# Kernel optimization log

Hardware: AMD Instinct MI355X
Metric: run time of the kernel (lower is better)

The kernel has to match this reference:

```python
import jax, jax.numpy as jnp
import numpy as np

EPS = 1e-5

def layer_norm(x, gamma, beta):
    mu = jnp.mean(x, axis=-1, keepdims=True)
    var = jnp.var(x, axis=-1, keepdims=True)
    return (x - mu) * jax.lax.rsqrt(var + EPS) * gamma + beta

def setup_inputs() -> dict:
    key = jax.random.key(0)
    ks = jax.random.split(key, 8)
    T, B, E, H, K = 2048, 2, 1024, 16, 64
    x = jax.random.normal(ks[0], (T, B, E), dtype=jnp.float32)
    # causal mask: 0 where allowed (s<=t), -1e9 where masked
    attn_mask = jnp.where(jnp.tril(jnp.ones((T, T), dtype=bool)), 0.0, -1e9).astype(jnp.float32)
    def xavier(k, shape, gain):
        fan_out, fan_in = shape
        std = gain * np.sqrt(2.0 / (fan_in + fan_out))
        return (jax.random.normal(k, shape, dtype=jnp.float32) * std)
    Wq = xavier(ks[1], (H * K, E), 1.0)
    Wk = xavier(ks[2], (K, E), 1.0)
    Wv = xavier(ks[3], (E, E), 1.0)
    return {
        'x': x, 'attn_mask': attn_mask,
        'Wq': Wq, 'bq': jnp.zeros((H * K,), jnp.float32),
        'Wk': Wk, 'bk': jnp.zeros((K,), jnp.float32),
        'Wv': Wv, 'bv': jnp.zeros((E,), jnp.float32),
        'k_gamma': jnp.ones((K,), jnp.float32), 'k_beta': jnp.zeros((K,), jnp.float32),
        'v_gamma': jnp.ones((E,), jnp.float32), 'v_beta': jnp.zeros((E,), jnp.float32),
    }

def reference(x, attn_mask, Wq, bq, Wk, bk, Wv, bv, k_gamma, k_beta, v_gamma, v_beta):
    T, B, E = x.shape
    K = Wk.shape[0]
    H = Wq.shape[0] // K
    q = (x @ Wq.T + bq).reshape(T, B, H, K)          # [T,B,H,K]
    k = layer_norm(x @ Wk.T + bk, k_gamma, k_beta)   # [T,B,K]
    v = layer_norm(x @ Wv.T + bv, v_gamma, v_beta)   # [T,B,E]
    # outer-product state per step, then causal cumulative sum.
    # einsum('ts,sbkd->tbkd', scaling*causal_mask, s) == cumsum over s<=t,
    # scaled per query position t by (t+1)^-0.5 (mask is causal lower-tri).
    outer = jnp.einsum('tbk,tbd->tbkd', k, v)        # [T,B,K,E]
    s = jnp.cumsum(outer, axis=0)
    scaling = jax.lax.rsqrt(jnp.arange(1, T + 1, dtype=x.dtype))
    s = s * scaling[:, None, None, None]
    qn = jnp.mean(jax.nn.softmax(q, axis=-1), axis=2)  # [T,B,K] (dropout_p=0, eval)
    attn = jnp.einsum('tbk,tbkd->tbd', qn, s)          # [T,B,E]
    return attn
```

## Files before the change

kernel.cpp:

```cpp
#include <hip/hip_runtime.h>
#include <math.h>

#define T_DIM 2048
#define B_DIM 2
#define E_DIM 1024
#define K_DIM 64
#define H_DIM 16
#define R_DIM (T_DIM * B_DIM)
#define WROWS 2176
#define NTILE 136

typedef __bf16 bf16x8 __attribute__((ext_vector_type(8)));
typedef __bf16 bf16x4 __attribute__((ext_vector_type(4)));
typedef float f32x4 __attribute__((ext_vector_type(4)));

__global__ __launch_bounds__(256) void cvt_x(const float* __restrict__ X,
                                             __bf16* __restrict__ O) {
    size_t g = ((size_t)blockIdx.x * 256 + threadIdx.x) * 8;
    float4 a = *(const float4*)&X[g];
    float4 b = *(const float4*)&X[g + 4];
    bf16x8 o;
    o[0] = (__bf16)a.x; o[1] = (__bf16)a.y; o[2] = (__bf16)a.z; o[3] = (__bf16)a.w;
    o[4] = (__bf16)b.x; o[5] = (__bf16)b.y; o[6] = (__bf16)b.z; o[7] = (__bf16)b.w;
    *(bf16x8*)&O[g] = o;
}

__global__ __launch_bounds__(256) void cvt_w(const float* __restrict__ Wq,
                                             const float* __restrict__ Wv,
                                             const float* __restrict__ Wk,
                                             __bf16* __restrict__ O) {
    const size_t nq = (size_t)1024 * 1024;
    const size_t nk = (size_t)64 * 1024;
    size_t g = ((size_t)blockIdx.x * 256 + threadIdx.x) * 8;
    bf16x8 o;
    if (g < 2 * nq + nk) {
        const float* src;
        size_t off;
        if (g < nq)          { src = Wq; off = g; }
        else if (g < 2 * nq) { src = Wv; off = g - nq; }
        else                 { src = Wk; off = g - 2 * nq; }
        float4 a = *(const float4*)&src[off];
        float4 b = *(const float4*)&src[off + 4];
        o[0] = (__bf16)a.x; o[1] = (__bf16)a.y; o[2] = (__bf16)a.z; o[3] = (__bf16)a.w;
        o[4] = (__bf16)b.x; o[5] = (__bf16)b.y; o[6] = (__bf16)b.z; o[7] = (__bf16)b.w;
    } else {
#pragma unroll
        for (int i = 0; i < 8; ++i) o[i] = (__bf16)0.f;
    }
    *(bf16x8*)&O[g] = o;
}

__global__ __launch_bounds__(256) void gemm_mfma(const __bf16* __restrict__ XB,
                                                 const __bf16* __restrict__ WB,
                                                 const float* __restrict__ bq,
                                                 const float* __restrict__ bv,
                                                 const float* __restrict__ bk,
                                                 float* __restrict__ Cq,
                                                 float* __restrict__ Cv,
                                                 float* __restrict__ Kr) {
    __shared__ __bf16 Als[128 * 32];
    __shared__ __bf16 Bls[128 * 32];
    const int tid = threadIdx.x;
    const int lane = tid & 63;
    const int w = tid >> 6;
    const int wm = (w & 1) * 64;
    const int wn = (w >> 1) * 64;
    const int rBase = blockIdx.x * 128;
    const int cBase = blockIdx.y * 128;

    const int c0 = tid, c1 = tid + 256;
    const __bf16* gA0 = XB + (size_t)(rBase + (c0 >> 2)) * E_DIM + (c0 & 3) * 8;
    const __bf16* gA1 = XB + (size_t)(rBase + (c1 >> 2)) * E_DIM + (c1 & 3) * 8;
    const __bf16* gB0 = WB + (size_t)(cBase + (c0 >> 2)) * E_DIM + (c0 & 3) * 8;
    const __bf16* gB1 = WB + (size_t)(cBase + (c1 >> 2)) * E_DIM + (c1 & 3) * 8;
    __bf16* lA0 = Als + c0 * 8;
    __bf16* lA1 = Als + c1 * 8;
    __bf16* lB0 = Bls + c0 * 8;
    __bf16* lB1 = Bls + c1 * 8;

    const int fr = lane & 15;
    const int fk = (lane >> 4) * 8;
    const __bf16* aF = Als + (wm + fr) * 32 + fk;
    const __bf16* bF = Bls + (wn + fr) * 32 + fk;

    f32x4 acc[4][4] = {};

    for (int kk = 0; kk < E_DIM; kk += 32) {
        __syncthreads();
        __builtin_amdgcn_global_load_lds(
            (const __attribute__((address_space(1))) void*)(gA0 + kk),
            (__attribute__((address_space(3))) void*)lA0, 16, 0, 0);
        __builtin_amdgcn_global_load_lds(
            (const __attribute__((address_space(1))) void*)(gA1 + kk),
            (__attribute__((address_space(3))) void*)lA1, 16, 0, 0);
        __builtin_amdgcn_global_load_lds(
            (const __attribute__((address_space(1))) void*)(gB0 + kk),
            (__attribute__((address_space(3))) void*)lB0, 16, 0, 0);
        __builtin_amdgcn_global_load_lds(
            (const __attribute__((address_space(1))) void*)(gB1 + kk),
            (__attribute__((address_space(3))) void*)lB1, 16, 0, 0);
        __syncthreads();

        bf16x8 af[4], bfr[4];
#pragma unroll
        for (int mt = 0; mt < 4; ++mt) af[mt] = *(const bf16x8*)(aF + mt * 16 * 32);
#pragma unroll
        for (int nt = 0; nt < 4; ++nt) bfr[nt] = *(const bf16x8*)(bF + nt * 16 * 32);
#pragma unroll
        for (int mt = 0; mt < 4; ++mt)
#pragma unroll
            for (int nt = 0; nt < 4; ++nt)
                acc[mt][nt] = __builtin_amdgcn_mfma_f32_16x16x32_bf16(
                    af[mt], bfr[nt], acc[mt][nt], 0, 0, 0);
    }

    const int row0 = rBase + wm + (lane >> 4) * 4;
    if (cBase < 2048) {
        const float* bias;
        float* Cout;
        int colBase;
        if (cBase < 1024) { bias = bq; Cout = Cq; colBase = cBase; }
        else              { bias = bv; Cout = Cv; colBase = cBase - 1024; }
        const int col0 = colBase + wn + (lane & 15);
#pragma unroll
        for (int mt = 0; mt < 4; ++mt)
#pragma unroll
            for (int nt = 0; nt < 4; ++nt) {
                int cc = col0 + nt * 16;
                float bb = bias[cc];
#pragma unroll
                for (int r = 0; r < 4; ++r)
                    Cout[(size_t)(row0 + mt * 16 + r) * E_DIM + cc] =
                        acc[mt][nt][r] + bb;
            }
    } else {
        const int col0 = wn + (lane & 15);
#pragma unroll
        for (int mt = 0; mt < 4; ++mt)
#pragma unroll
            for (int nt = 0; nt < 4; ++nt) {
                int cc = col0 + nt * 16;
                if (cc < 64) {
                    float bb = bk[cc];
#pragma unroll
                    for (int r = 0; r < 4; ++r)
                        Kr[(size_t)(row0 + mt * 16 + r) * K_DIM + cc] =
                            acc[mt][nt][r] + bb;
                }
            }
    }
}

__global__ __launch_bounds__(256) void softmax_mean(const float* __restrict__ Q,
                                                    __bf16* __restrict__ QNB) {
    const int r = blockIdx.x;
    const int tid = threadIdx.x;
    const int lane = tid & 63, wv = tid >> 6;
    float acc = 0.f;
#pragma unroll
    for (int h4 = 0; h4 < 4; ++h4) {
        int h = wv * 4 + h4;
        float v = Q[(size_t)r * 1024 + h * 64 + lane];
        float m = v;
#pragma unroll
        for (int off = 32; off; off >>= 1) m = fmaxf(m, __shfl_xor(m, off));
        float e = expf(v - m);
        float ssum = e;
#pragma unroll
        for (int off = 32; off; off >>= 1) ssum += __shfl_xor(ssum, off);
        acc += e / ssum;
    }
    __shared__ float red[4][64];
    red[wv][lane] = acc;
    __syncthreads();
    if (tid < 64) {
        float s = red[0][tid] + red[1][tid] + red[2][tid] + red[3][tid];
        int t = r >> 1, b = r & 1;
        QNB[((size_t)b * T_DIM + t) * K_DIM + tid] = (__bf16)(s * (1.f / 16.f));
    }
}

__global__ __launch_bounds__(64) void ln64(const float* __restrict__ Kraw,
                                           const float* __restrict__ gamma,
                                           const float* __restrict__ beta,
                                           __bf16* __restrict__ KNB) {
    const int r = blockIdx.x;
    const int lane = threadIdx.x;
    float v = Kraw[(size_t)r * K_DIM + lane];
    float s = v, s2 = v * v;
#pragma unroll
    for (int off = 32; off; off >>= 1) {
        s += __shfl_xor(s, off);
        s2 += __shfl_xor(s2, off);
    }
    float mean = s * (1.f / 64.f);
    float var = s2 * (1.f / 64.f) - mean * mean;
    float inv = rsqrtf(var + 1e-5f);
    int t = r >> 1, b = r & 1;
    KNB[((size_t)b * T_DIM + t) * K_DIM + lane] =
        (__bf16)((v - mean) * inv * gamma[lane] + beta[lane]);
}

__global__ __launch_bounds__(256) void vstats(const float* __restrict__ V,
                                              float2* __restrict__ ST) {
    const int r = blockIdx.x;
    const int tid = threadIdx.x;
    const int lane = tid & 63, wv = tid >> 6;
    float4 v = *(const float4*)&V[(size_t)r * E_DIM + tid * 4];
    float s = v.x + v.y + v.z + v.w;
    float s2 = v.x * v.x + v.y * v.y + v.z * v.z + v.w * v.w;
#pragma unroll
    for (int off = 32; off; off >>= 1) {
        s += __shfl_xor(s, off);
        s2 += __shfl_xor(s2, off);
    }
    __shared__ float red[2][4];
    if (lane == 0) { red[0][wv] = s; red[1][wv] = s2; }
    __syncthreads();
    if (tid == 0) {
        s = red[0][0] + red[0][1] + red[0][2] + red[0][3];
        s2 = red[1][0] + red[1][1] + red[1][2] + red[1][3];
        float mean = s * (1.f / 1024.f);
        float var = s2 * (1.f / 1024.f) - mean * mean;
        ST[r] = make_float2(mean, rsqrtf(var + 1e-5f));
    }
}

__global__ __launch_bounds__(256) void transpose_lnv(const float* __restrict__ V,
                                                     const float2* __restrict__ ST,
                                                     const float* __restrict__ gamma,
                                                     const float* __restrict__ beta,
                                                     __bf16* __restrict__ VT) {
    __shared__ float tile[64][65];
    const int tb = blockIdx.x, eb = blockIdx.y, b = blockIdx.z;
    const int tid = threadIdx.x;
#pragma unroll
    for (int j = 0; j < 4; ++j) {
        int idx = tid + j * 256;
        int tl = idx >> 4, e4 = idx & 15;
        int r = (tb * 64 + tl) * B_DIM + b;
        float2 st = ST[r];
        float4 v = *(const float4*)&V[(size_t)r * E_DIM + eb * 64 + e4 * 4];
        tile[tl][e4 * 4 + 0] = (v.x - st.x) * st.y;
        tile[tl][e4 * 4 + 1] = (v.y - st.x) * st.y;
        tile[tl][e4 * 4 + 2] = (v.z - st.x) * st.y;
        tile[tl][e4 * 4 + 3] = (v.w - st.x) * st.y;
    }
    __syncthreads();
#pragma unroll
    for (int j = 0; j < 4; ++j) {
        int idx = tid + j * 256;
        int e = idx >> 4, t4 = idx & 15;
        float g = gamma[eb * 64 + e], bb = beta[eb * 64 + e];
        bf16x4 o;
#pragma unroll
        for (int i = 0; i < 4; ++i) o[i] = (__bf16)(tile[t4 * 4 + i][e] * g + bb);
        *(bf16x4*)&VT[((size_t)b * E_DIM + eb * 64 + e) * T_DIM + tb * 64 + t4 * 4] = o;
    }
}

__global__ __launch_bounds__(256) void scoreK(const __bf16* __restrict__ QNB,
                                              const __bf16* __restrict__ KNB,
                                              __bf16* __restrict__ Pg) {
    __shared__ __bf16 qns[128 * 72];
    __shared__ __bf16 kns[128 * 72];
    const int tileId = blockIdx.x;
    const int b = blockIdx.y;
    int qt = 0, rem = tileId;
    while (rem > qt) { rem -= (qt + 1); ++qt; }
    const int st = rem;
    const int tid = threadIdx.x;
    const int lane = tid & 63;
    const int w = tid >> 6;
    const int qL = lane & 15;
    const int quad = lane >> 4;

    const __bf16* qsrc = QNB + ((size_t)b * T_DIM + qt * 128) * K_DIM;
    const __bf16* ksrc = KNB + ((size_t)b * T_DIM + st * 128) * K_DIM;
#pragma unroll
    for (int j = 0; j < 4; ++j) {
        int idx = tid + j * 256;
        int row = idx >> 3, k8 = idx & 7;
        *(bf16x8*)&qns[row * 72 + k8 * 8] = *(const bf16x8*)&qsrc[row * K_DIM + k8 * 8];
        *(bf16x8*)&kns[row * 72 + k8 * 8] = *(const bf16x8*)&ksrc[row * K_DIM + k8 * 8];
    }
    __syncthreads();

    f32x4 acc[8][2] = {};
#pragma unroll
    for (int kit = 0; kit < 2; ++kit) {
        bf16x8 bfr[2];
#pragma unroll
        for (int nt = 0; nt < 2; ++nt) {
            int q = w * 32 + nt * 16 + qL;
            bfr[nt] = *(const bf16x8*)&qns[q * 72 + kit * 32 + quad * 8];
        }
#pragma unroll
        for (int mt = 0; mt < 8; ++mt) {
            bf16x8 af = *(const bf16x8*)&kns[(mt * 16 + qL) * 72 + kit * 32 + quad * 8];
#pragma unroll
            for (int nt = 0; nt < 2; ++nt)
                acc[mt][nt] = __builtin_amdgcn_mfma_f32_16x16x32_bf16(
                    af, bfr[nt], acc[mt][nt], 0, 0, 0);
        }
    }
    __bf16* pb = Pg + ((size_t)(b * NTILE + tileId)) * 128 * 128;
#pragma unroll
    for (int mt = 0; mt < 8; ++mt)
#pragma unroll
        for (int nt = 0; nt < 2; ++nt) {
            int q = w * 32 + nt * 16 + qL;
            int s0 = mt * 16 + quad * 4;
            bf16x4 o;
#pragma unroll
            for (int r = 0; r < 4; ++r) {
                float val = acc[mt][nt][r];
                if (qt == st && (s0 + r) > q) val = 0.f;
                o[r] = (__bf16)val;
            }
            *(bf16x4*)&pb[(size_t)q * 128 + s0] = o;
        }
}

__global__ __launch_bounds__(256) void flashPV(const __bf16* __restrict__ Pg,
                                               const __bf16* __restrict__ VT,
                                               float* __restrict__ OUT) {
    __shared__ __align__(16) __bf16 vts[64 * 136];
    __shared__ __align__(16) __bf16 ps[128 * 136];
    const int p = blockIdx.x;
    const int es = blockIdx.y;
    const int b = blockIdx.z;
    const int tid = threadIdx.x;
    const int lane = tid & 63;
    const int w = tid >> 6;
    const int qL = lane & 15;
    const int quad = lane >> 4;

    for (int ph = 0; ph < 2; ++ph) {
        const int qt = ph ? (15 - p) : p;
        const int tileBase = qt * (qt + 1) / 2;
        f32x4 acc[4][2] = {};

        for (int st = 0; st <= qt; ++st) {
            __syncthreads();
#pragma unroll
            for (int j = 0; j < 4; ++j) {
                int idx = tid + j * 256;
                int e = idx >> 4, sc = idx & 15;
                *(bf16x8*)&vts[e * 136 + sc * 8] =
                    *(const bf16x8*)&VT[((size_t)b * E_DIM + es * 64 + e) * T_DIM +
                                        st * 128 + sc * 8];
            }
            const __bf16* pb = Pg + ((size_t)(b * NTILE + tileBase + st)) * 128 * 128;
#pragma unroll
            for (int j = 0; j < 8; ++j) {
                int idx = tid + j * 256;
                int q = idx >> 4, sc = idx & 15;
                *(bf16x8*)&ps[q * 136 + sc * 8] = *(const bf16x8*)&pb[q * 128 + sc * 8];
            }
            __syncthreads();
#pragma unroll
            for (int kit = 0; kit < 4; ++kit) {
                bf16x8 bfr[2];
#pragma unroll
                for (int nt = 0; nt < 2; ++nt) {
                    int q = w * 32 + nt * 16 + qL;
                    bfr[nt] = *(const bf16x8*)&ps[q * 136 + kit * 32 + quad * 8];
                }
#pragma unroll
                for (int mt = 0; mt < 4; ++mt) {
                    bf16x8 af = *(const bf16x8*)&vts[(mt * 16 + qL) * 136 + kit * 32 + quad * 8];
#pragma unroll
                    for (int nt = 0; nt < 2; ++nt)
                        acc[mt][nt] = __builtin_amdgcn_mfma_f32_16x16x32_bf16(
                            af, bfr[nt], acc[mt][nt], 0, 0, 0);
                }
            }
        }
        __syncthreads();

        float* tb = (float*)vts + w * 640;
#pragma unroll
        for (int mt = 0; mt < 4; ++mt) {
#pragma unroll
            for (int nt = 0; nt < 2; ++nt)
                *(f32x4*)&tb[(nt * 16 + qL) * 20 + quad * 4] = acc[mt][nt];
#pragma unroll
            for (int j = 0; j < 2; ++j) {
                int fid = lane + j * 64;
                int q = fid >> 2, e4 = fid & 3;
                float4 val = *(const float4*)&tb[q * 20 + e4 * 4];
                int t = qt * 128 + w * 32 + q;
                float sca = rsqrtf((float)(t + 1));
                float4 r = {val.x * sca, val.y * sca, val.z * sca, val.w * sca};
                *(float4*)&OUT[((size_t)t * B_DIM + b) * E_DIM + es * 64 + mt * 16 + e4 * 4] = r;
            }
        }
    }
}

extern "C" void kernel_launch(void* const* d_in, const int* in_sizes, int n_in,
                              void* d_out, int out_size, void* d_ws,
                              size_t ws_size, hipStream_t stream) {
    const float* x = (const float*)d_in[0];
    const float* Wq = (const float*)d_in[2];
    const float* bq = (const float*)d_in[3];
    const float* Wk = (const float*)d_in[4];
    const float* bk = (const float*)d_in[5];
    const float* Wv = (const float*)d_in[6];
    const float* bv = (const float*)d_in[7];
    const float* kg = (const float*)d_in[8];
    const float* kb = (const float*)d_in[9];
    const float* vg = (const float*)d_in[10];
    const float* vb = (const float*)d_in[11];
    float* out = (float*)d_out;

    float* ws = (float*)d_ws;
    float* qraw = ws;
    float* v = ws + (size_t)4 * 1024 * 1024;
    float* kraw = ws + (size_t)8 * 1024 * 1024;
    __bf16* xb = (__bf16*)(kraw + 256 * 1024);
    __bf16* wb = xb + (size_t)4 * 1024 * 1024;
    __bf16* qnb = wb + (size_t)WROWS * 1024;
    __bf16* knb = qnb + 256 * 1024;
    float2* stats = (float2*)(knb + 256 * 1024);
    __bf16* Pg = (__bf16*)qraw;
    __bf16* vbT = xb;

    cvt_x<<<dim3(2048), 256, 0, stream>>>(x, xb);
    cvt_w<<<dim3(WROWS * 1024 / 8 / 256), 256, 0, stream>>>(Wq, Wv, Wk, wb);
    gemm_mfma<<<dim3(32, 17), 256, 0, stream>>>(xb, wb, bq, bv, bk, qraw, v, kraw);
    softmax_mean<<<dim3(R_DIM), 256, 0, stream>>>(qraw, qnb);
    ln64<<<dim3(R_DIM), 64, 0, stream>>>(kraw, kg, kb, knb);
    vstats<<<dim3(R_DIM), 256, 0, stream>>>(v, stats);
    transpose_lnv<<<dim3(T_DIM / 64, E_DIM / 64, B_DIM), 256, 0, stream>>>(
        v, stats, vg, vb, vbT);
    scoreK<<<dim3(NTILE, B_DIM), 256, 0, stream>>>(qnb, knb, Pg);
    flashPV<<<dim3(8, 16, B_DIM), 256, 0, stream>>>(Pg, vbT, out);
}
```

Measured before the change: 191.9 us.

## Fuse conversion and row-wise kernels, store Q/V GEMM outputs as bf16

Merges the x and weight bf16 conversion kernels into one launch, and merges softmax-mean, K layernorm and V statistics into a single per-row kernel. The GEMM now writes the Q and V projections as bf16 instead of fp32, which halves the intermediate traffic read by the row and transpose kernels. This removes several launches and some memory bandwidth. In exchange, Q logits and V values are rounded to bf16 before the softmax and layernorm statistics, which slightly reduces accuracy.

```diff
diff --git a/kernel.cpp b/kernel.cpp
--- a/kernel.cpp
+++ b/kernel.cpp
@@ -14,40 +14,40 @@
 typedef __bf16 bf16x4 __attribute__((ext_vector_type(4)));
 typedef float f32x4 __attribute__((ext_vector_type(4)));
 
-__global__ __launch_bounds__(256) void cvt_x(const float* __restrict__ X,
-                                             __bf16* __restrict__ O) {
-    size_t g = ((size_t)blockIdx.x * 256 + threadIdx.x) * 8;
-    float4 a = *(const float4*)&X[g];
-    float4 b = *(const float4*)&X[g + 4];
-    bf16x8 o;
-    o[0] = (__bf16)a.x; o[1] = (__bf16)a.y; o[2] = (__bf16)a.z; o[3] = (__bf16)a.w;
-    o[4] = (__bf16)b.x; o[5] = (__bf16)b.y; o[6] = (__bf16)b.z; o[7] = (__bf16)b.w;
-    *(bf16x8*)&O[g] = o;
-}
-
-__global__ __launch_bounds__(256) void cvt_w(const float* __restrict__ Wq,
-                                             const float* __restrict__ Wv,
-                                             const float* __restrict__ Wk,
-                                             __bf16* __restrict__ O) {
+__global__ __launch_bounds__(256) void cvt_all(const float* __restrict__ X,
+                                               const float* __restrict__ Wq,
+                                               const float* __restrict__ Wv,
+                                               const float* __restrict__ Wk,
+                                               __bf16* __restrict__ XB,
+                                               __bf16* __restrict__ WB) {
     const size_t nq = (size_t)1024 * 1024;
     const size_t nk = (size_t)64 * 1024;
-    size_t g = ((size_t)blockIdx.x * 256 + threadIdx.x) * 8;
     bf16x8 o;
-    if (g < 2 * nq + nk) {
-        const float* src;
-        size_t off;
-        if (g < nq)          { src = Wq; off = g; }
-        else if (g < 2 * nq) { src = Wv; off = g - nq; }
-        else                 { src = Wk; off = g - 2 * nq; }
-        float4 a = *(const float4*)&src[off];
-        float4 b = *(const float4*)&src[off + 4];
+    if (blockIdx.x < 2048) {
+        size_t g = ((size_t)blockIdx.x * 256 + threadIdx.x) * 8;
+        float4 a = *(const float4*)&X[g];
+        float4 b = *(const float4*)&X[g + 4];
         o[0] = (__bf16)a.x; o[1] = (__bf16)a.y; o[2] = (__bf16)a.z; o[3] = (__bf16)a.w;
         o[4] = (__bf16)b.x; o[5] = (__bf16)b.y; o[6] = (__bf16)b.z; o[7] = (__bf16)b.w;
+        *(bf16x8*)&XB[g] = o;
     } else {
-#pragma unroll
-        for (int i = 0; i < 8; ++i) o[i] = (__bf16)0.f;
-    }
-    *(bf16x8*)&O[g] = o;
+        size_t g = ((size_t)(blockIdx.x - 2048) * 256 + threadIdx.x) * 8;
+        if (g < 2 * nq + nk) {
+            const float* src;
+            size_t off;
+            if (g < nq)          { src = Wq; off = g; }
+            else if (g < 2 * nq) { src = Wv; off = g - nq; }
+            else                 { src = Wk; off = g - 2 * nq; }
+            float4 a = *(const float4*)&src[off];
+            float4 b = *(const float4*)&src[off + 4];
+            o[0] = (__bf16)a.x; o[1] = (__bf16)a.y; o[2] = (__bf16)a.z; o[3] = (__bf16)a.w;
+            o[4] = (__bf16)b.x; o[5] = (__bf16)b.y; o[6] = (__bf16)b.z; o[7] = (__bf16)b.w;
+        } else {
+#pragma unroll
+            for (int i = 0; i < 8; ++i) o[i] = (__bf16)0.f;
+        }
+        *(bf16x8*)&WB[g] = o;
+    }
 }
 
 __global__ __launch_bounds__(256) void gemm_mfma(const __bf16* __restrict__ XB,
@@ -55,8 +55,8 @@
                                                  const float* __restrict__ bq,
                                                  const float* __restrict__ bv,
                                                  const float* __restrict__ bk,
-                                                 float* __restrict__ Cq,
-                                                 float* __restrict__ Cv,
+                                                 __bf16* __restrict__ Qb,
+                                                 __bf16* __restrict__ Vb,
                                                  float* __restrict__ Kr) {
     __shared__ __bf16 Als[128 * 32];
     __shared__ __bf16 Bls[128 * 32];
@@ -117,10 +117,10 @@
     const int row0 = rBase + wm + (lane >> 4) * 4;
     if (cBase < 2048) {
         const float* bias;
-        float* Cout;
+        __bf16* Cout;
         int colBase;
-        if (cBase < 1024) { bias = bq; Cout = Cq; colBase = cBase; }
-        else              { bias = bv; Cout = Cv; colBase = cBase - 1024; }
+        if (cBase < 1024) { bias = bq; Cout = Qb; colBase = cBase; }
+        else              { bias = bv; Cout = Vb; colBase = cBase - 1024; }
         const int col0 = colBase + wn + (lane & 15);
 #pragma unroll
         for (int mt = 0; mt < 4; ++mt)
@@ -131,7 +131,7 @@
 #pragma unroll
                 for (int r = 0; r < 4; ++r)
                     Cout[(size_t)(row0 + mt * 16 + r) * E_DIM + cc] =
-                        acc[mt][nt][r] + bb;
+                        (__bf16)(acc[mt][nt][r] + bb);
             }
     } else {
         const int col0 = wn + (lane & 15);
@@ -151,82 +151,77 @@
     }
 }
 
-__global__ __launch_bounds__(256) void softmax_mean(const float* __restrict__ Q,
-                                                    __bf16* __restrict__ QNB) {
-    const int r = blockIdx.x;
-    const int tid = threadIdx.x;
-    const int lane = tid & 63, wv = tid >> 6;
-    float acc = 0.f;
-#pragma unroll
-    for (int h4 = 0; h4 < 4; ++h4) {
-        int h = wv * 4 + h4;
-        float v = Q[(size_t)r * 1024 + h * 64 + lane];
-        float m = v;
-#pragma unroll
-        for (int off = 32; off; off >>= 1) m = fmaxf(m, __shfl_xor(m, off));
-        float e = expf(v - m);
-        float ssum = e;
-#pragma unroll
-        for (int off = 32; off; off >>= 1) ssum += __shfl_xor(ssum, off);
-        acc += e / ssum;
-    }
-    __shared__ float red[4][64];
-    red[wv][lane] = acc;
-    __syncthreads();
-    if (tid < 64) {
-        float s = red[0][tid] + red[1][tid] + red[2][tid] + red[3][tid];
-        int t = r >> 1, b = r & 1;
-        QNB[((size_t)b * T_DIM + t) * K_DIM + tid] = (__bf16)(s * (1.f / 16.f));
-    }
-}
-
-__global__ __launch_bounds__(64) void ln64(const float* __restrict__ Kraw,
-                                           const float* __restrict__ gamma,
-                                           const float* __restrict__ beta,
-                                           __bf16* __restrict__ KNB) {
-    const int r = blockIdx.x;
-    const int lane = threadIdx.x;
-    float v = Kraw[(size_t)r * K_DIM + lane];
-    float s = v, s2 = v * v;
-#pragma unroll
-    for (int off = 32; off; off >>= 1) {
-        s += __shfl_xor(s, off);
-        s2 += __shfl_xor(s2, off);
-    }
-    float mean = s * (1.f / 64.f);
-    float var = s2 * (1.f / 64.f) - mean * mean;
-    float inv = rsqrtf(var + 1e-5f);
-    int t = r >> 1, b = r & 1;
-    KNB[((size_t)b * T_DIM + t) * K_DIM + lane] =
-        (__bf16)((v - mean) * inv * gamma[lane] + beta[lane]);
-}
-
-__global__ __launch_bounds__(256) void vstats(const float* __restrict__ V,
+__global__ __launch_bounds__(256) void rowops(const __bf16* __restrict__ Qb,
+                                              const float* __restrict__ Kraw,
+                                              const __bf16* __restrict__ Vb,
+                                              const float* __restrict__ kg,
+                                              const float* __restrict__ kb,
+                                              __bf16* __restrict__ QNB,
+                                              __bf16* __restrict__ KNB,
                                               float2* __restrict__ ST) {
     const int r = blockIdx.x;
     const int tid = threadIdx.x;
     const int lane = tid & 63, wv = tid >> 6;
-    float4 v = *(const float4*)&V[(size_t)r * E_DIM + tid * 4];
-    float s = v.x + v.y + v.z + v.w;
-    float s2 = v.x * v.x + v.y * v.y + v.z * v.z + v.w * v.w;
-#pragma unroll
-    for (int off = 32; off; off >>= 1) {
-        s += __shfl_xor(s, off);
-        s2 += __shfl_xor(s2, off);
-    }
-    __shared__ float red[2][4];
-    if (lane == 0) { red[0][wv] = s; red[1][wv] = s2; }
+    const int t = r >> 1, b = r & 1;
+    __shared__ float redq[4][64];
+    __shared__ float redv[2][4];
+
+    float acc = 0.f;
+#pragma unroll
+    for (int h4 = 0; h4 < 4; ++h4) {
+        int h = wv * 4 + h4;
+        float v = (float)Qb[(size_t)r * 1024 + h * 64 + lane];
+        float m = v;
+#pragma unroll
+        for (int off = 32; off; off >>= 1) m = fmaxf(m, __shfl_xor(m, off));
+        float e = expf(v - m);
+        float ssum = e;
+#pragma unroll
+        for (int off = 32; off; off >>= 1) ssum += __shfl_xor(ssum, off);
+        acc += e / ssum;
+    }
+    redq[wv][lane] = acc;
+
+    {
+        bf16x4 v4 = *(const bf16x4*)&Vb[(size_t)r * 1024 + tid * 4];
+        float a = (float)v4[0], c = (float)v4[1], d = (float)v4[2], e = (float)v4[3];
+        float s = a + c + d + e;
+        float s2 = a * a + c * c + d * d + e * e;
+#pragma unroll
+        for (int off = 32; off; off >>= 1) {
+            s += __shfl_xor(s, off);
+            s2 += __shfl_xor(s2, off);
+        }
+        if (lane == 0) { redv[0][wv] = s; redv[1][wv] = s2; }
+    }
     __syncthreads();
-    if (tid == 0) {
-        s = red[0][0] + red[0][1] + red[0][2] + red[0][3];
-        s2 = red[1][0] + red[1][1] + red[1][2] + red[1][3];
+
+    if (tid < 64) {
+        float s = redq[0][tid] + redq[1][tid] + redq[2][tid] + redq[3][tid];
+        QNB[((size_t)b * T_DIM + t) * K_DIM + tid] = (__bf16)(s * (1.f / 16.f));
+    } else if (tid < 128) {
+        float v = Kraw[(size_t)r * K_DIM + lane];
+        float s = v, s2 = v * v;
+#pragma unroll
+        for (int off = 32; off; off >>= 1) {
+            s += __shfl_xor(s, off);
+            s2 += __shfl_xor(s2, off);
+        }
+        float mean = s * (1.f / 64.f);
+        float var = s2 * (1.f / 64.f) - mean * mean;
+        float inv = rsqrtf(var + 1e-5f);
+        KNB[((size_t)b * T_DIM + t) * K_DIM + lane] =
+            (__bf16)((v - mean) * inv * kg[lane] + kb[lane]);
+    } else if (tid == 128) {
+        float s = redv[0][0] + redv[0][1] + redv[0][2] + redv[0][3];
+        float s2 = redv[1][0] + redv[1][1] + redv[1][2] + redv[1][3];
         float mean = s * (1.f / 1024.f);
         float var = s2 * (1.f / 1024.f) - mean * mean;
         ST[r] = make_float2(mean, rsqrtf(var + 1e-5f));
     }
 }
 
-__global__ __launch_bounds__(256) void transpose_lnv(const float* __restrict__ V,
+__global__ __launch_bounds__(256) void transpose_lnv(const __bf16* __restrict__ VB,
                                                      const float2* __restrict__ ST,
                                                      const float* __restrict__ gamma,
                                                      const float* __restrict__ beta,
@@ -235,16 +230,15 @@
     const int tb = blockIdx.x, eb = blockIdx.y, b = blockIdx.z;
     const int tid = threadIdx.x;
 #pragma unroll
-    for (int j = 0; j < 4; ++j) {
+    for (int j = 0; j < 2; ++j) {
         int idx = tid + j * 256;
-        int tl = idx >> 4, e4 = idx & 15;
+        int tl = idx >> 3, e8 = idx & 7;
         int r = (tb * 64 + tl) * B_DIM + b;
         float2 st = ST[r];
-        float4 v = *(const float4*)&V[(size_t)r * E_DIM + eb * 64 + e4 * 4];
-        tile[tl][e4 * 4 + 0] = (v.x - st.x) * st.y;
-        tile[tl][e4 * 4 + 1] = (v.y - st.x) * st.y;
-        tile[tl][e4 * 4 + 2] = (v.z - st.x) * st.y;
-        tile[tl][e4 * 4 + 3] = (v.w - st.x) * st.y;
+        bf16x8 v = *(const bf16x8*)&VB[(size_t)r * E_DIM + eb * 64 + e8 * 8];
+#pragma unroll
+        for (int i = 0; i < 8; ++i)
+            tile[tl][e8 * 8 + i] = ((float)v[i] - st.x) * st.y;
     }
     __syncthreads();
 #pragma unroll
@@ -415,26 +409,24 @@
     const float* vb = (const float*)d_in[11];
     float* out = (float*)d_out;
 
-    float* ws = (float*)d_ws;
-    float* qraw = ws;
-    float* v = ws + (size_t)4 * 1024 * 1024;
-    float* kraw = ws + (size_t)8 * 1024 * 1024;
-    __bf16* xb = (__bf16*)(kraw + 256 * 1024);
-    __bf16* wb = xb + (size_t)4 * 1024 * 1024;
-    __bf16* qnb = wb + (size_t)WROWS * 1024;
-    __bf16* knb = qnb + 256 * 1024;
-    float2* stats = (float2*)(knb + 256 * 1024);
-    __bf16* Pg = (__bf16*)qraw;
+    char* base = (char*)d_ws;
+    const size_t MB = 1024 * 1024;
+    __bf16* qb    = (__bf16*)(base + 0);
+    __bf16* vbuf  = (__bf16*)(base + 8 * MB);
+    float*  kraw  = (float*)(base + 16 * MB);
+    __bf16* xb    = (__bf16*)(base + 17 * MB);
+    __bf16* wb    = (__bf16*)(base + 25 * MB);
+    __bf16* qnb   = (__bf16*)(base + 30 * MB);
+    __bf16* knb   = (__bf16*)(base + 31 * MB);
+    float2* stats = (float2*)(base + 32 * MB);
+    __bf16* Pg  = (__bf16*)(base + 0);
     __bf16* vbT = xb;
 
-    cvt_x<<<dim3(2048), 256, 0, stream>>>(x, xb);
-    cvt_w<<<dim3(WROWS * 1024 / 8 / 256), 256, 0, stream>>>(Wq, Wv, Wk, wb);
-    gemm_mfma<<<dim3(32, 17), 256, 0, stream>>>(xb, wb, bq, bv, bk, qraw, v, kraw);
-    softmax_mean<<<dim3(R_DIM), 256, 0, stream>>>(qraw, qnb);
-    ln64<<<dim3(R_DIM), 64, 0, stream>>>(kraw, kg, kb, knb);
-    vstats<<<dim3(R_DIM), 256, 0, stream>>>(v, stats);
+    cvt_all<<<dim3(2048 + WROWS * 1024 / 2048), 256, 0, stream>>>(x, Wq, Wv, Wk, xb, wb);
+    gemm_mfma<<<dim3(32, 17), 256, 0, stream>>>(xb, wb, bq, bv, bk, qb, vbuf, kraw);
+    rowops<<<dim3(R_DIM), 256, 0, stream>>>(qb, kraw, vbuf, kg, kb, qnb, knb, stats);
     transpose_lnv<<<dim3(T_DIM / 64, E_DIM / 64, B_DIM), 256, 0, stream>>>(
-        v, stats, vg, vb, vbT);
+        vbuf, stats, vg, vb, vbT);
     scoreK<<<dim3(NTILE, B_DIM), 256, 0, stream>>>(qnb, knb, Pg);
     flashPV<<<dim3(8, 16, B_DIM), 256, 0, stream>>>(Pg, vbT, out);
 }
```

After: 186.6 us. 2.7% less time.
